# Performance work log

Measured on AMD Instinct MI355X. Metric: run time of the kernel, lower is better.

The kernel has to match this reference:

```python
import jax, jax.numpy as jnp
import numpy as np

BN, N, M, P_OBS = 65536, 15, 6, 6

def _spd(k, b, n, scale=0.1):
    L = scale * jax.random.normal(k, (b, n, n), dtype=jnp.float32)
    return L @ L.mT + 0.1 * jnp.eye(n, dtype=jnp.float32)

def setup_inputs() -> dict:
    key = jax.random.key(0)
    ks = jax.random.split(key, 12)
    I_n = jnp.eye(N, dtype=jnp.float32)
    state = jax.random.normal(ks[0], (BN, N), dtype=jnp.float32)
    obs = jax.random.normal(ks[1], (BN, P_OBS), dtype=jnp.float32)
    u = jax.random.normal(ks[2], (BN, M), dtype=jnp.float32)
    P = _spd(ks[3], BN, N)
    A = I_n + 0.01 * jax.random.normal(ks[4], (BN, N, N), dtype=jnp.float32)
    B_mat = 0.1 * jax.random.normal(ks[5], (BN, N, M), dtype=jnp.float32)
    C = 0.1 * jax.random.normal(ks[6], (BN, P_OBS, N), dtype=jnp.float32)
    D = 0.1 * jax.random.normal(ks[7], (BN, P_OBS, M), dtype=jnp.float32)
    c1 = jax.random.normal(ks[8], (BN, N), dtype=jnp.float32)
    c2 = jax.random.normal(ks[9], (BN, P_OBS), dtype=jnp.float32)
    Q = _spd(ks[10], BN, M)
    R = _spd(ks[11], BN, P_OBS)
    return {"state": state, "obs": obs, "u": u, "P": P, "A": A, "B_mat": B_mat,
            "C": C, "D": D, "c1": c1, "c2": c2, "Q": Q, "R": R}

def reference(state, obs, u, P, A, B_mat, C, D, c1, c2, Q, R):
    # Linearized system: f(x,u) = A x + B u + c1 ; g(x,u) = C x + D u + c2
    I = jnp.eye(P.shape[-1], dtype=P.dtype)
    # priori state: xp = f(state, u)
    xp = jnp.einsum('bij,bj->bi', A, state) + jnp.einsum('bij,bj->bi', B_mat, u) + c1
    # priori covariance: P- = A P A^T + B Q B^T
    Pp = A @ P @ A.mT + B_mat @ Q @ B_mat.mT
    # Kalman gain: K = P- C^T pinv(C P- C^T + R)
    S = C @ Pp @ C.mT + R                       # [B, p, p]
    K = Pp @ C.mT @ jnp.linalg.pinv(S)          # [B, n, p]
    # innovation: e = obs - g(state, u)  (observation at previous state, as in source)
    e = obs - (jnp.einsum('bij,bj->bi', C, state) + jnp.einsum('bij,bj->bi', D, u) + c2)
    xp = xp + jnp.einsum('bij,bj->bi', K, e)
    # Joseph-form posterior covariance
    IKC = I - K @ C
    Pn = IKC @ Pp @ IKC.mT + K @ R @ K.mT
    return xp, Pn
```

## Files before the change

### kernel.cpp

```cpp
#include <hip/hip_runtime.h>

#define XOR16(v)     __shfl_xor((v), 16, 64)
#define FENCE() asm volatile("" ::: "memory")
#define SB() __builtin_amdgcn_sched_barrier(0)

#define STR    1236
#define OFF_M1    0
#define OFF_M2  300
#define OFF_C   600
#define OFF_S4  696
#define OFF_Q   816
#define OFF_R   864
#define OFF_VX  912
#define OFF_VU  928
#define OFF_M3  936

__device__ __forceinline__ float dot15(const float* Lr, const float* v) {
    float4 x0 = *(const float4*)(Lr);
    float4 x1 = *(const float4*)(Lr + 4);
    float4 x2 = *(const float4*)(Lr + 8);
    float4 x3 = *(const float4*)(Lr + 12);
    return v[0]*x0.x + v[1]*x0.y + v[2]*x0.z + v[3]*x0.w
         + v[4]*x1.x + v[5]*x1.y + v[6]*x1.z + v[7]*x1.w
         + v[8]*x2.x + v[9]*x2.y + v[10]*x2.z + v[11]*x2.w
         + v[12]*x3.x + v[13]*x3.y + v[14]*x3.z;
}
__device__ __forceinline__ void rd15(const float* Lr, float* v) {
    float4 x0 = *(const float4*)(Lr);
    float4 x1 = *(const float4*)(Lr + 4);
    float4 x2 = *(const float4*)(Lr + 8);
    float4 x3 = *(const float4*)(Lr + 12);
    v[0]=x0.x; v[1]=x0.y; v[2]=x0.z; v[3]=x0.w;
    v[4]=x1.x; v[5]=x1.y; v[6]=x1.z; v[7]=x1.w;
    v[8]=x2.x; v[9]=x2.y; v[10]=x2.z; v[11]=x2.w;
    v[12]=x3.x; v[13]=x3.y; v[14]=x3.z;
}
__device__ __forceinline__ float dot8(const float* Lr, const float* v) {
    float4 x0 = *(const float4*)(Lr);
    float4 x1 = *(const float4*)(Lr + 4);
    return v[0]*x0.x + v[1]*x0.y + v[2]*x0.z + v[3]*x0.w
         + v[4]*x1.x + v[5]*x1.y + v[6]*x1.z + v[7]*x1.w;
}
__device__ __forceinline__ void rd8(const float* Lr, float* v) {
    float4 x0 = *(const float4*)(Lr);
    float4 x1 = *(const float4*)(Lr + 4);
    v[0]=x0.x; v[1]=x0.y; v[2]=x0.z; v[3]=x0.w;
    v[4]=x1.x; v[5]=x1.y; v[6]=x1.z; v[7]=x1.w;
}
__device__ __forceinline__ void axpy8(const float* Lr, float s, float* acc) {
    float4 x0 = *(const float4*)(Lr);
    float4 x1 = *(const float4*)(Lr + 4);
    acc[0]+=s*x0.x; acc[1]+=s*x0.y; acc[2]+=s*x0.z; acc[3]+=s*x0.w;
    acc[4]+=s*x1.x; acc[5]+=s*x1.y; acc[6]+=s*x1.z; acc[7]+=s*x1.w;
}
__device__ __forceinline__ void wrow8(float* Lr, const float* v) {
    *(float4*)(Lr)     = make_float4(v[0],v[1],v[2],v[3]);
    *(float4*)(Lr + 4) = make_float4(v[4],v[5],v[6],v[7]);
}
__device__ __forceinline__ float dot6(const float* Lr, const float* v) {
    float4 x0 = *(const float4*)(Lr);
    float2 x1 = *(const float2*)(Lr + 4);
    return v[0]*x0.x + v[1]*x0.y + v[2]*x0.z + v[3]*x0.w + v[4]*x1.x + v[5]*x1.y;
}
__device__ __forceinline__ void rd6(const float* Lr, float* v) {
    float4 x0 = *(const float4*)(Lr);
    float2 x1 = *(const float2*)(Lr + 4);
    v[0]=x0.x; v[1]=x0.y; v[2]=x0.z; v[3]=x0.w; v[4]=x1.x; v[5]=x1.y;
}
__device__ __forceinline__ void wrow6(float* Lr, const float* v) {
    *(float4*)(Lr)     = make_float4(v[0],v[1],v[2],v[3]);
    *(float2*)(Lr + 4) = make_float2(v[4],v[5]);
}

__global__
__attribute__((amdgpu_flat_work_group_size(64, 64)))
__attribute__((amdgpu_waves_per_eu(2, 4)))
void ekf_kernel(
    const float* __restrict__ g_state, const float* __restrict__ g_obs,
    const float* __restrict__ g_u,     const float* __restrict__ g_P,
    const float* __restrict__ g_A,     const float* __restrict__ g_B,
    const float* __restrict__ g_C,     const float* __restrict__ g_D,
    const float* __restrict__ g_c1,    const float* __restrict__ g_c2,
    const float* __restrict__ g_Q,     const float* __restrict__ g_R,
    float* __restrict__ o_xp, float* __restrict__ o_Pn, int bn)
{
    __shared__ __align__(16) float lds[2 * STR];
    const int tid = threadIdx.x;
    const int ib0 = blockIdx.x * 2;
    const int nIt = min(2, bn - ib0);

    const int g   = tid >> 5;
    const int s   = tid & 31;
    const int r   = s & 15;
    const int h   = s >> 4;
    const int j0  = 8 * h;
    const int itc = ib0 + ((g < nIt) ? g : (nIt - 1));
    const int rc  = r < 15 ? r : 14;
    const int rc6 = r < 6 ? r : 5;
    float* L = lds + g * STR;

    const float* gp = g_P + (size_t)ib0 * 225;
    const float* ga = g_A + (size_t)ib0 * 225;
    const float* gc = g_C + (size_t)ib0 * 90;
    const float* gb = g_B + (size_t)ib0 * 90;
    const float* gq = g_Q + (size_t)ib0 * 36;
    const float* gr = g_R + (size_t)ib0 * 36;
    const float* gs = g_state + (size_t)ib0 * 15;
    const float* gu = g_u + (size_t)ib0 * 6;
    const int limPA = nIt * 225, limCB = nIt * 90, limQR = nIt * 36;
    const int limS = nIt * 15, limU = nIt * 6;

    float vP[8], vA[8], vC[3], vB[3], vQ[2], vR[2], vS, vU;
    #pragma unroll
    for (int t = 0; t < 8; ++t) {
        int i = min(tid + t * 64, limPA - 1);
        vP[t] = gp[i]; vA[t] = ga[i];
    }
    #pragma unroll
    for (int t = 0; t < 3; ++t) {
        int i = min(tid + t * 64, limCB - 1);
        vC[t] = gc[i]; vB[t] = gb[i];
    }
    #pragma unroll
    for (int t = 0; t < 2; ++t) {
        int i = min(tid + t * 64, limQR - 1);
        vQ[t] = gq[i]; vR[t] = gr[i];
    }
    vS = gs[min(tid, limS - 1)];
    vU = gu[min(tid, limU - 1)];
    float c1v  = g_c1[(size_t)itc * 15 + rc];
    float obsv = g_obs[(size_t)itc * 6 + rc6];
    float c2v  = g_c2[(size_t)itc * 6 + rc6];
    const float* Db = g_D + (size_t)itc * 36 + rc6 * 6;
    float dd0 = Db[0], dd1 = Db[1], dd2 = Db[2], dd3 = Db[3], dd4 = Db[4], dd5 = Db[5];

    #pragma unroll
    for (int t = 0; t < 8; ++t) {
        int i = tid + t * 64;
        if (i < 450) {
            int it = i / 225, idx = i - it * 225;
            int rw = idx / 15, j = idx - rw * 15;
            lds[it * STR + OFF_M1 + rw * 20 + j] = vP[t];
            lds[it * STR + OFF_M2 + rw * 20 + j] = vA[t];
        }
    }
    #pragma unroll
    for (int t = 0; t < 3; ++t) {
        int i = tid + t * 64;
        if (i < 180) {
            int it = i / 90, idx = i - it * 90;
            int rw = idx / 15, j = idx - rw * 15;
            lds[it * STR + OFF_C + rw * 16 + j] = vC[t];
            int rb = idx / 6, jb = idx - rb * 6;
            lds[it * STR + OFF_S4 + rb * 8 + jb] = vB[t];
        }
    }
    #pragma unroll
    for (int t = 0; t < 2; ++t) {
        int i = tid + t * 64;
        if (i < 72) {
            int it = i / 36, idx = i - it * 36;
            int rw = idx / 6, j = idx - rw * 6;
            lds[it * STR + OFF_Q + rw * 8 + j] = vQ[t];
            lds[it * STR + OFF_R + rw * 8 + j] = vR[t];
        }
    }
    if (tid < 30) { int it = tid / 15, rw = tid - it * 15; lds[it * STR + OFF_VX + rw] = vS; }
    if (tid < 12) { int it = tid / 6,  rw = tid - it * 6;  lds[it * STR + OFF_VU + rw] = vU; }
    if (r < 15) { L[OFF_M1 + r * 20 + 15] = 0.f; L[OFF_M2 + r * 20 + 15] = 0.f; }
    if (s < 6)  L[OFF_C + s * 16 + 15] = 0.f;
    if (s == 15) L[OFF_VX + 15] = 0.f;
    FENCE(); SB();

    float xp;
    {
        float xh[8]; rd8(L + OFF_VX + j0, xh);
        float u6[6]; rd6(L + OFF_VU, u6);
        float xpp =  dot8(L + OFF_M2 + rc * 20 + j0, xh);
        float evp = -dot8(L + OFF_C + rc6 * 16 + j0, xh);
        if (h == 0) {
            xpp += c1v + dot6(L + OFF_S4 + rc * 8, u6);
            evp += obsv - c2v
                 - (dd0*u6[0] + dd1*u6[1] + dd2*u6[2]
                  + dd3*u6[3] + dd4*u6[4] + dd5*u6[5]);
        }
        xp = xpp + XOR16(xpp);
        float ev = evp + XOR16(evp);
        FENCE();
        if (h == 0 && r < 6) L[OFF_VX + r] = ev;
        FENCE();
    }
    SB();

    float pp8[8];
    {
        float af[15]; rd15(L + OFF_M2 + rc * 20, af);
        float y8[8];
        #pragma unroll
        for (int j = 0; j < 8; ++j) y8[j] = 0.f;
        #define YK(k) axpy8(L + OFF_M1 + (k)*20 + j0, af[(k)], y8)
        YK(0); YK(1); YK(2); YK(3); YK(4); SB();
        YK(5); YK(6); YK(7); YK(8); YK(9); SB();
        YK(10); YK(11); YK(12); YK(13); YK(14); SB();
        FENCE();
        if (r < 15) wrow8(L + OFF_M3 + rc * 20 + j0, y8);
        FENCE(); SB();
    }
    {
        float yf[15]; rd15(L + OFF_M3 + rc * 20, yf);
        #define PPJ(j) pp8[(j)] = ((j0 + (j)) < 15) ? dot15(L + OFF_M2 + (j0 + (j))*20, yf) : 0.f
        PPJ(0); PPJ(1); PPJ(2); PPJ(3); SB();
        PPJ(4); PPJ(5); PPJ(6); PPJ(7); SB();
    }
    {
        float bf[6]; rd6(L + OFF_S4 + rc * 8, bf);
        float z[6];
        #pragma unroll
        for (int j = 0; j < 6; ++j) z[j] = 0.f;
        #define ZK(k) do { float qk[6]; rd6(L + OFF_Q + (k)*8, qk); \
            z[0]+=bf[(k)]*qk[0]; z[1]+=bf[(k)]*qk[1]; z[2]+=bf[(k)]*qk[2]; \
            z[3]+=bf[(k)]*qk[3]; z[4]+=bf[(k)]*qk[4]; z[5]+=bf[(k)]*qk[5]; } while(0)
        ZK(0); ZK(1); ZK(2); SB(); ZK(3); ZK(4); ZK(5); SB();
        #define PBJ(j) if ((j0 + (j)) < 15) pp8[(j)] += dot6(L + OFF_S4 + (j0 + (j))*8, z)
        PBJ(0); PBJ(1); PBJ(2); PBJ(3); SB(); PBJ(4); PBJ(5); PBJ(6); PBJ(7); SB();
    }
    FENCE();
    if (r < 15) wrow8(L + OFF_M1 + rc * 20 + j0, pp8);
    FENCE(); SB();

    float ppct[6];
    {
        #define PCJ(c) ppct[(c)] = dot8(L + OFF_C + (c)*16 + j0, pp8)
        PCJ(0); PCJ(1); PCJ(2); SB(); PCJ(3); PCJ(4); PCJ(5); SB();
        #pragma unroll
        for (int c = 0; c < 6; ++c) ppct[c] += XOR16(ppct[c]);
    }
    FENCE();
    if (h == 0 && r < 15) wrow6(L + OFF_M3 + r * 20, ppct);
    FENCE(); SB();

    float kk[6];
    {
        float sm[6];
        #pragma unroll
        for (int c = 0; c < 6; ++c) sm[c] = 0.f;
        {
            float ch[8]; rd8(L + OFF_C + rc6 * 16 + j0, ch);
            #define SAK(k) do { float pr[6]; rd6(L + OFF_M3 + min(j0 + (k), 14)*20, pr); \
                float cv = ch[(k)]; \
                sm[0]+=cv*pr[0]; sm[1]+=cv*pr[1]; sm[2]+=cv*pr[2]; \
                sm[3]+=cv*pr[3]; sm[4]+=cv*pr[4]; sm[5]+=cv*pr[5]; } while(0)
            SAK(0); SAK(1); SAK(2); SAK(3); SB();
            SAK(4); SAK(5); SAK(6); SAK(7); SB();
        }
        #pragma unroll
        for (int c = 0; c < 6; ++c) sm[c] += XOR16(sm[c]);
        if (h == 0 && r < 6) {
            float rr6[6]; rd6(L + OFF_R + r * 8, rr6);
            float srow[6];
            #pragma unroll
            for (int c = 0; c < 6; ++c) srow[c] = sm[c] + rr6[c];
            wrow6(L + OFF_Q + r * 8, srow);
        }
        FENCE(); SB();

        float r0[6], r1[6], r2[6], r3[6], r4[6], r5[6];
        rd6(L + OFF_Q + 0*8, r0); rd6(L + OFF_Q + 1*8, r1); rd6(L + OFF_Q + 2*8, r2); SB();
        rd6(L + OFF_Q + 3*8, r3); rd6(L + OFF_Q + 4*8, r4); rd6(L + OFF_Q + 5*8, r5); SB();

        float l00 = sqrtf(r0[0]);                 float i0 = 1.f / l00;
        float l10 = r1[0]*i0, l20 = r2[0]*i0, l30 = r3[0]*i0, l40 = r4[0]*i0, l50 = r5[0]*i0;
        float l11 = sqrtf(r1[1] - l10*l10);       float i1 = 1.f / l11;
        float l21 = (r2[1] - l20*l10)*i1;
        float l31 = (r3[1] - l30*l10)*i1;
        float l41 = (r4[1] - l40*l10)*i1;
        float l51 = (r5[1] - l50*l10)*i1;
        float l22 = sqrtf(r2[2] - l20*l20 - l21*l21); float i2 = 1.f / l22;
        float l32 = (r3[2] - l30*l20 - l31*l21)*i2;
        float l42 = (r4[2] - l40*l20 - l41*l21)*i2;
        float l52 = (r5[2] - l50*l20 - l51*l21)*i2;
        float l33 = sqrtf(r3[3] - l30*l30 - l31*l31 - l32*l32); float i3 = 1.f / l33;
        float l43 = (r4[3] - l40*l30 - l41*l31 - l42*l32)*i3;
        float l53 = (r5[3] - l50*l30 - l51*l31 - l52*l32)*i3;
        float l44 = sqrtf(r4[4] - l40*l40 - l41*l41 - l42*l42 - l43*l43); float i4 = 1.f / l44;
        float l54 = (r5[4] - l50*l40 - l51*l41 - l52*l42 - l53*l43)*i4;
        float l55 = sqrtf(r5[5] - l50*l50 - l51*l51 - l52*l52 - l53*l53 - l54*l54);
        float i5 = 1.f / l55;

        float y0 =  ppct[0]*i0;
        float y1 = (ppct[1] - l10*y0)*i1;
        float y2 = (ppct[2] - l20*y0 - l21*y1)*i2;
        float y3 = (ppct[3] - l30*y0 - l31*y1 - l32*y2)*i3;
        float y4 = (ppct[4] - l40*y0 - l41*y1 - l42*y2 - l43*y3)*i4;
        float y5 = (ppct[5] - l50*y0 - l51*y1 - l52*y2 - l53*y3 - l54*y4)*i5;
        kk[5] =  y5*i5;
        kk[4] = (y4 - l54*kk[5])*i4;
        kk[3] = (y3 - l43*kk[4] - l53*kk[5])*i3;
        kk[2] = (y2 - l32*kk[3] - l42*kk[4] - l52*kk[5])*i2;
        kk[1] = (y1 - l21*kk[2] - l31*kk[3] - l41*kk[4] - l51*kk[5])*i1;
        kk[0] = (y0 - l10*kk[1] - l20*kk[2] - l30*kk[3] - l40*kk[4] - l50*kk[5])*i0;
    }
    FENCE();
    if (h == 0 && r < 15) wrow6(L + OFF_M3 + r * 20 + 8, kk);
    FENCE();
    {
        float e6[6]; rd6(L + OFF_VX, e6);
        xp += kk[0]*e6[0] + kk[1]*e6[1] + kk[2]*e6[2]
            + kk[3]*e6[3] + kk[4]*e6[4] + kk[5]*e6[5];
    }
    SB();

    float pn8[8];
    {
        float t38[8];
        #define T3J(j) do { float pr[6]; rd6(L + OFF_M3 + min(j0 + (j), 14)*20, pr); \
            t38[(j)] = pp8[(j)] - (kk[0]*pr[0]+kk[1]*pr[1]+kk[2]*pr[2] \
                                  +kk[3]*pr[3]+kk[4]*pr[4]+kk[5]*pr[5]); } while(0)
        T3J(0); T3J(1); T3J(2); T3J(3); SB();
        T3J(4); T3J(5); T3J(6); T3J(7); SB();
        if (j0 + 7 >= 15) t38[7] = 0.f;

        float w[6];
        #define GJ(c) w[(c)] = dot8(L + OFF_C + (c)*16 + j0, t38)
        GJ(0); GJ(1); GJ(2); SB(); GJ(3); GJ(4); GJ(5); SB();
        #pragma unroll
        for (int c = 0; c < 6; ++c) w[c] = -(w[c] + XOR16(w[c]));

        #define KRK(k) do { float rk[6]; rd6(L + OFF_R + (k)*8, rk); \
            w[0]+=kk[(k)]*rk[0]; w[1]+=kk[(k)]*rk[1]; w[2]+=kk[(k)]*rk[2]; \
            w[3]+=kk[(k)]*rk[3]; w[4]+=kk[(k)]*rk[4]; w[5]+=kk[(k)]*rk[5]; } while(0)
        KRK(0); KRK(1); KRK(2); SB(); KRK(3); KRK(4); KRK(5); SB();

        #define PNJ(j) do { float krow[6]; rd6(L + OFF_M3 + min(j0 + (j), 14)*20 + 8, krow); \
            pn8[(j)] = t38[(j)] + (w[0]*krow[0]+w[1]*krow[1]+w[2]*krow[2] \
                                  +w[3]*krow[3]+w[4]*krow[4]+w[5]*krow[5]); } while(0)
        PNJ(0); PNJ(1); PNJ(2); PNJ(3); SB();
        PNJ(4); PNJ(5); PNJ(6); PNJ(7); SB();
        if (j0 + 7 >= 15) pn8[7] = 0.f;
    }

    FENCE();
    if (r < 15) {
        wrow8(L + OFF_M1 + rc * 20 + j0, pn8);
        if (h == 0) L[OFF_S4 + r * 8 + 6] = xp;
    }
    FENCE(); SB();

    {
        float* gpn = o_Pn + (size_t)ib0 * 225;
        float sP[8];
        #pragma unroll
        for (int t = 0; t < 8; ++t) {
            int i = min(tid + t * 64, 449);
            int it = i / 225, idx = i - it * 225;
            int rw = idx / 15, j = idx - rw * 15;
            sP[t] = lds[it * STR + OFF_M1 + rw * 20 + j];
        }
        #pragma unroll
        for (int t = 0; t < 8; ++t) {
            int i = tid + t * 64;
            if (i < limPA) gpn[i] = sP[t];
        }
        float* gxp = o_xp + (size_t)ib0 * 15;
        if (tid < limS) {
            int it = tid / 15, rw = tid - it * 15;
            gxp[tid] = lds[it * STR + OFF_S4 + rw * 8 + 6];
        }
    }
}

extern "C" void kernel_launch(void* const* d_in, const int* in_sizes, int n_in,
                              void* d_out, int out_size, void* d_ws, size_t ws_size,
                              hipStream_t stream) {
    const float* g_state = (const float*)d_in[0];
    const float* g_obs   = (const float*)d_in[1];
    const float* g_u     = (const float*)d_in[2];
    const float* g_P     = (const float*)d_in[3];
    const float* g_A     = (const float*)d_in[4];
    const float* g_B     = (const float*)d_in[5];
    const float* g_C     = (const float*)d_in[6];
    const float* g_D     = (const float*)d_in[7];
    const float* g_c1    = (const float*)d_in[8];
    const float* g_c2    = (const float*)d_in[9];
    const float* g_Q     = (const float*)d_in[10];
    const float* g_R     = (const float*)d_in[11];

    const int bn = in_sizes[0] / 15;
    float* o_xp = (float*)d_out;
    float* o_pn = o_xp + (size_t)bn * 15;

    const int blocks = (bn + 1) / 2;
    ekf_kernel<<<blocks, 64, 0, stream>>>(
        g_state, g_obs, g_u, g_P, g_A, g_B, g_C, g_D, g_c1, g_c2, g_Q, g_R,
        o_xp, o_pn, bn);
}
```

Measured before the change: 110.6 us.

## Compute priori covariance with bf16 MFMA using augmented [A|B] and blockdiag(P,Q)

Replaces the scalar FP32 LDS loops for A P A^T + B Q B^T with bf16 MFMA 16x16x32 instructions. It packs [A|B] and blockdiag(P,Q) into zero-padded bf16 tiles in shared memory and forms both products as a single augmented matmul pair. The aim is to cut VALU and LDS traffic in the dominant covariance-propagation stage. In exchange it grows the LDS footprint, adds conversion and transpose round-trips, and lowers the precision of Pp to bf16 inputs, which may loosen numerical accuracy.

```diff
diff --git a/kernel.cpp b/kernel.cpp
--- a/kernel.cpp
+++ b/kernel.cpp
@@ -4,36 +4,25 @@
 #define FENCE() asm volatile("" ::: "memory")
 #define SB() __builtin_amdgcn_sched_barrier(0)
 
-#define STR    1236
+#define STR    1932
 #define OFF_M1    0
-#define OFF_M2  300
-#define OFF_C   600
-#define OFF_S4  696
-#define OFF_Q   816
-#define OFF_R   864
-#define OFF_VX  912
-#define OFF_VU  928
-#define OFF_M3  936
-
-__device__ __forceinline__ float dot15(const float* Lr, const float* v) {
-    float4 x0 = *(const float4*)(Lr);
-    float4 x1 = *(const float4*)(Lr + 4);
-    float4 x2 = *(const float4*)(Lr + 8);
-    float4 x3 = *(const float4*)(Lr + 12);
-    return v[0]*x0.x + v[1]*x0.y + v[2]*x0.z + v[3]*x0.w
-         + v[4]*x1.x + v[5]*x1.y + v[6]*x1.z + v[7]*x1.w
-         + v[8]*x2.x + v[9]*x2.y + v[10]*x2.z + v[11]*x2.w
-         + v[12]*x3.x + v[13]*x3.y + v[14]*x3.z;
-}
-__device__ __forceinline__ void rd15(const float* Lr, float* v) {
-    float4 x0 = *(const float4*)(Lr);
-    float4 x1 = *(const float4*)(Lr + 4);
-    float4 x2 = *(const float4*)(Lr + 8);
-    float4 x3 = *(const float4*)(Lr + 12);
-    v[0]=x0.x; v[1]=x0.y; v[2]=x0.z; v[3]=x0.w;
-    v[4]=x1.x; v[5]=x1.y; v[6]=x1.z; v[7]=x1.w;
-    v[8]=x2.x; v[9]=x2.y; v[10]=x2.z; v[11]=x2.w;
-    v[12]=x3.x; v[13]=x3.y; v[14]=x3.z;
+#define OFF_M2  320
+#define OFF_C   620
+#define OFF_S4  716
+#define OFF_R   836
+#define OFF_VX  884
+#define OFF_VU  900
+#define OFF_GB  908
+#define OFF_HB  1228
+#define OFF_SS  1868
+
+using bf16x8 = __attribute__((ext_vector_type(8))) short;
+using f32x4  = __attribute__((ext_vector_type(4))) float;
+
+__device__ __forceinline__ unsigned short f2bf(float f) {
+    union { float f; unsigned u; } v; v.f = f;
+    unsigned r = v.u + 0x7FFFu + ((v.u >> 16) & 1u);
+    return (unsigned short)(r >> 16);
 }
 __device__ __forceinline__ float dot8(const float* Lr, const float* v) {
     float4 x0 = *(const float4*)(Lr);
@@ -47,16 +36,6 @@
     v[0]=x0.x; v[1]=x0.y; v[2]=x0.z; v[3]=x0.w;
     v[4]=x1.x; v[5]=x1.y; v[6]=x1.z; v[7]=x1.w;
 }
-__device__ __forceinline__ void axpy8(const float* Lr, float s, float* acc) {
-    float4 x0 = *(const float4*)(Lr);
-    float4 x1 = *(const float4*)(Lr + 4);
-    acc[0]+=s*x0.x; acc[1]+=s*x0.y; acc[2]+=s*x0.z; acc[3]+=s*x0.w;
-    acc[4]+=s*x1.x; acc[5]+=s*x1.y; acc[6]+=s*x1.z; acc[7]+=s*x1.w;
-}
-__device__ __forceinline__ void wrow8(float* Lr, const float* v) {
-    *(float4*)(Lr)     = make_float4(v[0],v[1],v[2],v[3]);
-    *(float4*)(Lr + 4) = make_float4(v[4],v[5],v[6],v[7]);
-}
 __device__ __forceinline__ float dot6(const float* Lr, const float* v) {
     float4 x0 = *(const float4*)(Lr);
     float2 x1 = *(const float2*)(Lr + 4);
@@ -70,6 +49,10 @@
 __device__ __forceinline__ void wrow6(float* Lr, const float* v) {
     *(float4*)(Lr)     = make_float4(v[0],v[1],v[2],v[3]);
     *(float2*)(Lr + 4) = make_float2(v[4],v[5]);
+}
+__device__ __forceinline__ void wrow8(float* Lr, const float* v) {
+    *(float4*)(Lr)     = make_float4(v[0],v[1],v[2],v[3]);
+    *(float4*)(Lr + 4) = make_float4(v[4],v[5],v[6],v[7]);
 }
 
 __global__
@@ -135,12 +118,20 @@
     float dd0 = Db[0], dd1 = Db[1], dd2 = Db[2], dd3 = Db[3], dd4 = Db[4], dd5 = Db[5];
 
     #pragma unroll
+    for (int g2 = 0; g2 < 2; ++g2) {
+        #pragma unroll
+        for (int t = 0; t < 4; ++t)
+            *(float4*)(lds + g2 * STR + OFF_GB + t * 256 + tid * 4)
+                = make_float4(0.f, 0.f, 0.f, 0.f);
+    }
+    FENCE();
+
+    #pragma unroll
     for (int t = 0; t < 8; ++t) {
         int i = tid + t * 64;
         if (i < 450) {
             int it = i / 225, idx = i - it * 225;
             int rw = idx / 15, j = idx - rw * 15;
-            lds[it * STR + OFF_M1 + rw * 20 + j] = vP[t];
             lds[it * STR + OFF_M2 + rw * 20 + j] = vA[t];
         }
     }
@@ -161,15 +152,45 @@
         if (i < 72) {
             int it = i / 36, idx = i - it * 36;
             int rw = idx / 6, j = idx - rw * 6;
-            lds[it * STR + OFF_Q + rw * 8 + j] = vQ[t];
             lds[it * STR + OFF_R + rw * 8 + j] = vR[t];
         }
     }
     if (tid < 30) { int it = tid / 15, rw = tid - it * 15; lds[it * STR + OFF_VX + rw] = vS; }
     if (tid < 12) { int it = tid / 6,  rw = tid - it * 6;  lds[it * STR + OFF_VU + rw] = vU; }
-    if (r < 15) { L[OFF_M1 + r * 20 + 15] = 0.f; L[OFF_M2 + r * 20 + 15] = 0.f; }
     if (s < 6)  L[OFF_C + s * 16 + 15] = 0.f;
     if (s == 15) L[OFF_VX + 15] = 0.f;
+
+    {
+        unsigned short* lb = (unsigned short*)lds;
+        #pragma unroll
+        for (int t = 0; t < 8; ++t) {
+            int i = tid + t * 64;
+            if (i < 450) {
+                int it = i / 225, idx = i - it * 225;
+                int rw = idx / 15, j = idx - rw * 15;
+                lb[(it * STR + OFF_GB) * 2 + rw * 40 + j] = f2bf(vA[t]);
+                lb[(it * STR + OFF_HB) * 2 + rw * 40 + j] = f2bf(vP[t]);
+            }
+        }
+        #pragma unroll
+        for (int t = 0; t < 3; ++t) {
+            int i = tid + t * 64;
+            if (i < 180) {
+                int it = i / 90, idx = i - it * 90;
+                int rb = idx / 6, jb = idx - rb * 6;
+                lb[(it * STR + OFF_GB) * 2 + rb * 40 + 16 + jb] = f2bf(vB[t]);
+            }
+        }
+        #pragma unroll
+        for (int t = 0; t < 2; ++t) {
+            int i = tid + t * 64;
+            if (i < 72) {
+                int it = i / 36, idx = i - it * 36;
+                int rq = idx / 6, cq = idx - rq * 6;
+                lb[(it * STR + OFF_HB) * 2 + (16 + rq) * 40 + 16 + cq] = f2bf(vQ[t]);
+            }
+        }
+    }
     FENCE(); SB();
 
     float xp;
@@ -192,42 +213,47 @@
     }
     SB();
 
+    const int q  = tid >> 4;
+    const int cL = tid & 15;
+    {
+        char* lb = (char*)lds;
+        bf16x8 ga0  = *(bf16x8*)(lb + (0*STR + OFF_GB)*4 + cL*80 + q*16);
+        bf16x8 ga1  = *(bf16x8*)(lb + (1*STR + OFF_GB)*4 + cL*80 + q*16);
+        bf16x8 hb00 = *(bf16x8*)(lb + (0*STR + OFF_HB)*4 + cL*80 + q*16);
+        bf16x8 hb01 = *(bf16x8*)(lb + (0*STR + OFF_HB)*4 + (16+cL)*80 + q*16);
+        bf16x8 hb10 = *(bf16x8*)(lb + (1*STR + OFF_HB)*4 + cL*80 + q*16);
+        bf16x8 hb11 = *(bf16x8*)(lb + (1*STR + OFF_HB)*4 + (16+cL)*80 + q*16);
+        f32x4 z = {0.f, 0.f, 0.f, 0.f};
+        f32x4 y00 = __builtin_amdgcn_mfma_f32_16x16x32_bf16(ga0, hb00, z, 0, 0, 0);
+        f32x4 y01 = __builtin_amdgcn_mfma_f32_16x16x32_bf16(ga0, hb01, z, 0, 0, 0);
+        f32x4 y10 = __builtin_amdgcn_mfma_f32_16x16x32_bf16(ga1, hb10, z, 0, 0, 0);
+        f32x4 y11 = __builtin_amdgcn_mfma_f32_16x16x32_bf16(ga1, hb11, z, 0, 0, 0);
+        FENCE();
+        *(f32x4*)(lds + 0*STR + OFF_HB + cL*20 + 4*q)        = y00;
+        *(f32x4*)(lds + 0*STR + OFF_HB + (16 + cL)*20 + 4*q) = y01;
+        *(f32x4*)(lds + 1*STR + OFF_HB + cL*20 + 4*q)        = y10;
+        *(f32x4*)(lds + 1*STR + OFF_HB + (16 + cL)*20 + 4*q) = y11;
+        FENCE(); SB();
+        bf16x8 ya0, ya1;
+        #pragma unroll
+        for (int j = 0; j < 8; ++j) {
+            float a0 = lds[0*STR + OFF_HB + (8*q + j)*20 + cL];
+            float a1 = lds[1*STR + OFF_HB + (8*q + j)*20 + cL];
+            ya0[j] = (short)f2bf(a0);
+            ya1[j] = (short)f2bf(a1);
+        }
+        SB();
+        f32x4 pp0 = __builtin_amdgcn_mfma_f32_16x16x32_bf16(ya0, ga0, z, 0, 0, 0);
+        f32x4 pp1 = __builtin_amdgcn_mfma_f32_16x16x32_bf16(ya1, ga1, z, 0, 0, 0);
+        FENCE();
+        *(f32x4*)(lds + 0*STR + OFF_M1 + cL*20 + 4*q) = pp0;
+        *(f32x4*)(lds + 1*STR + OFF_M1 + cL*20 + 4*q) = pp1;
+        FENCE(); SB();
+    }
+
     float pp8[8];
-    {
-        float af[15]; rd15(L + OFF_M2 + rc * 20, af);
-        float y8[8];
-        #pragma unroll
-        for (int j = 0; j < 8; ++j) y8[j] = 0.f;
-        #define YK(k) axpy8(L + OFF_M1 + (k)*20 + j0, af[(k)], y8)
-        YK(0); YK(1); YK(2); YK(3); YK(4); SB();
-        YK(5); YK(6); YK(7); YK(8); YK(9); SB();
-        YK(10); YK(11); YK(12); YK(13); YK(14); SB();
-        FENCE();
-        if (r < 15) wrow8(L + OFF_M3 + rc * 20 + j0, y8);
-        FENCE(); SB();
-    }
-    {
-        float yf[15]; rd15(L + OFF_M3 + rc * 20, yf);
-        #define PPJ(j) pp8[(j)] = ((j0 + (j)) < 15) ? dot15(L + OFF_M2 + (j0 + (j))*20, yf) : 0.f
-        PPJ(0); PPJ(1); PPJ(2); PPJ(3); SB();
-        PPJ(4); PPJ(5); PPJ(6); PPJ(7); SB();
-    }
-    {
-        float bf[6]; rd6(L + OFF_S4 + rc * 8, bf);
-        float z[6];
-        #pragma unroll
-        for (int j = 0; j < 6; ++j) z[j] = 0.f;
-        #define ZK(k) do { float qk[6]; rd6(L + OFF_Q + (k)*8, qk); \
-            z[0]+=bf[(k)]*qk[0]; z[1]+=bf[(k)]*qk[1]; z[2]+=bf[(k)]*qk[2]; \
-            z[3]+=bf[(k)]*qk[3]; z[4]+=bf[(k)]*qk[4]; z[5]+=bf[(k)]*qk[5]; } while(0)
-        ZK(0); ZK(1); ZK(2); SB(); ZK(3); ZK(4); ZK(5); SB();
-        #define PBJ(j) if ((j0 + (j)) < 15) pp8[(j)] += dot6(L + OFF_S4 + (j0 + (j))*8, z)
-        PBJ(0); PBJ(1); PBJ(2); PBJ(3); SB(); PBJ(4); PBJ(5); PBJ(6); PBJ(7); SB();
-    }
-    FENCE();
-    if (r < 15) wrow8(L + OFF_M1 + rc * 20 + j0, pp8);
-    FENCE(); SB();
-
+    rd8(L + OFF_M1 + rc * 20 + j0, pp8);
+    SB();
     float ppct[6];
     {
         #define PCJ(c) ppct[(c)] = dot8(L + OFF_C + (c)*16 + j0, pp8)
@@ -236,7 +262,7 @@
         for (int c = 0; c < 6; ++c) ppct[c] += XOR16(ppct[c]);
     }
     FENCE();
-    if (h == 0 && r < 15) wrow6(L + OFF_M3 + r * 20, ppct);
+    if (h == 0 && r < 15) wrow6(L + OFF_M2 + r * 20, ppct);
     FENCE(); SB();
 
     float kk[6];
@@ -246,7 +272,7 @@
         for (int c = 0; c < 6; ++c) sm[c] = 0.f;
         {
             float ch[8]; rd8(L + OFF_C + rc6 * 16 + j0, ch);
-            #define SAK(k) do { float pr[6]; rd6(L + OFF_M3 + min(j0 + (k), 14)*20, pr); \
+            #define SAK(k) do { float pr[6]; rd6(L + OFF_M2 + min(j0 + (k), 14)*20, pr); \
                 float cv = ch[(k)]; \
                 sm[0]+=cv*pr[0]; sm[1]+=cv*pr[1]; sm[2]+=cv*pr[2]; \
                 sm[3]+=cv*pr[3]; sm[4]+=cv*pr[4]; sm[5]+=cv*pr[5]; } while(0)
@@ -260,13 +286,13 @@
             float srow[6];
             #pragma unroll
             for (int c = 0; c < 6; ++c) srow[c] = sm[c] + rr6[c];
-            wrow6(L + OFF_Q + r * 8, srow);
+            wrow6(L + OFF_SS + r * 8, srow);
         }
         FENCE(); SB();
 
         float r0[6], r1[6], r2[6], r3[6], r4[6], r5[6];
-        rd6(L + OFF_Q + 0*8, r0); rd6(L + OFF_Q + 1*8, r1); rd6(L + OFF_Q + 2*8, r2); SB();
-        rd6(L + OFF_Q + 3*8, r3); rd6(L + OFF_Q + 4*8, r4); rd6(L + OFF_Q + 5*8, r5); SB();
+        rd6(L + OFF_SS + 0*8, r0); rd6(L + OFF_SS + 1*8, r1); rd6(L + OFF_SS + 2*8, r2); SB();
+        rd6(L + OFF_SS + 3*8, r3); rd6(L + OFF_SS + 4*8, r4); rd6(L + OFF_SS + 5*8, r5); SB();
 
         float l00 = sqrtf(r0[0]);                 float i0 = 1.f / l00;
         float l10 = r1[0]*i0, l20 = r2[0]*i0, l30 = r3[0]*i0, l40 = r4[0]*i0, l50 = r5[0]*i0;
@@ -301,7 +327,7 @@
         kk[0] = (y0 - l10*kk[1] - l20*kk[2] - l30*kk[3] - l40*kk[4] - l50*kk[5])*i0;
     }
     FENCE();
-    if (h == 0 && r < 15) wrow6(L + OFF_M3 + r * 20 + 8, kk);
+    if (h == 0 && r < 15) wrow6(L + OFF_M2 + r * 20 + 8, kk);
     FENCE();
     {
         float e6[6]; rd6(L + OFF_VX, e6);
@@ -313,7 +339,7 @@
     float pn8[8];
     {
         float t38[8];
-        #define T3J(j) do { float pr[6]; rd6(L + OFF_M3 + min(j0 + (j), 14)*20, pr); \
+        #define T3J(j) do { float pr[6]; rd6(L + OFF_M2 + min(j0 + (j), 14)*20, pr); \
             t38[(j)] = pp8[(j)] - (kk[0]*pr[0]+kk[1]*pr[1]+kk[2]*pr[2] \
                                   +kk[3]*pr[3]+kk[4]*pr[4]+kk[5]*pr[5]); } while(0)
         T3J(0); T3J(1); T3J(2); T3J(3); SB();
@@ -331,7 +357,7 @@
             w[3]+=kk[(k)]*rk[3]; w[4]+=kk[(k)]*rk[4]; w[5]+=kk[(k)]*rk[5]; } while(0)
         KRK(0); KRK(1); KRK(2); SB(); KRK(3); KRK(4); KRK(5); SB();
 
-        #define PNJ(j) do { float krow[6]; rd6(L + OFF_M3 + min(j0 + (j), 14)*20 + 8, krow); \
+        #define PNJ(j) do { float krow[6]; rd6(L + OFF_M2 + min(j0 + (j), 14)*20 + 8, krow); \
             pn8[(j)] = t38[(j)] + (w[0]*krow[0]+w[1]*krow[1]+w[2]*krow[2] \
                                   +w[3]*krow[3]+w[4]*krow[4]+w[5]*krow[5]); } while(0)
         PNJ(0); PNJ(1); PNJ(2); PNJ(3); SB();
```

Measured after the change: 111.0 us. About the same (+0.4%).
